# Performance work log

Hardware: AMD Instinct MI355X
Metric: run time of the kernel (lower is better)

The kernel has to match this reference:

```python
import jax, jax.numpy as jnp
import numpy as np

WH, WW = 8, 8
N = WH * WW
DIM = 128
NUM_HEADS = 4
HEAD_DIM = DIM // NUM_HEADS
SCALE = HEAD_DIM ** -0.5


def _relative_position_index():
    coords = np.stack(np.meshgrid(np.arange(WH), np.arange(WW), indexing='ij'))  # (2, Wh, Ww)
    flat = coords.reshape(2, -1)  # (2, N)
    rel = flat[:, :, None] - flat[:, None, :]  # (2, N, N)
    rel = rel.transpose(1, 2, 0)  # (N, N, 2)
    rel[:, :, 0] += WH - 1
    rel[:, :, 1] += WW - 1
    rel[:, :, 0] *= 2 * WW - 1
    return rel.sum(-1)  # (N, N) int

REL_IDX = _relative_position_index()


def setup_inputs() -> dict:
    key = jax.random.key(0)
    ks = jax.random.split(key, 7)
    B_ = 4096
    nW = 64
    table_size = (2 * WH - 1) * (2 * WW - 1)  # 225
    return {
        'x': jax.random.normal(ks[0], (B_, N, DIM), dtype=jnp.float32),
        'mask': jax.random.normal(ks[1], (nW, N, N), dtype=jnp.float32),
        'qkv_w': jax.random.normal(ks[2], (3 * DIM, DIM), dtype=jnp.float32) * 0.02,
        'qkv_b': jnp.zeros((3 * DIM,), dtype=jnp.float32),
        'proj_w': jax.random.normal(ks[3], (DIM, DIM), dtype=jnp.float32) * 0.02,
        'proj_b': jnp.zeros((DIM,), dtype=jnp.float32),
        'bias_table': jax.random.normal(ks[4], (table_size, NUM_HEADS), dtype=jnp.float32) * 0.02,
    }


def reference(x, mask, qkv_w, qkv_b, proj_w, proj_b, bias_table):
    B_, n, C = x.shape
    nW = mask.shape[0]
    qkv = x @ qkv_w.T + qkv_b  # (B_, N, 3C)
    qkv = qkv.reshape(B_, n, 3, NUM_HEADS, HEAD_DIM)
    q = qkv[:, :, 0] * SCALE  # (B_, N, H, hd)
    k = qkv[:, :, 1]
    v = qkv[:, :, 2]
    attn = jnp.einsum('bihd,bjhd->bhij', q, k)  # (B_, H, N, N)
    rel_bias = bias_table[REL_IDX.reshape(-1)].reshape(n, n, NUM_HEADS)
    attn = attn + rel_bias.transpose(2, 0, 1)[None]  # broadcast over B_
    attn = attn.reshape(B_ // nW, nW, NUM_HEADS, n, n) + mask[None, :, None]
    attn = attn.reshape(B_, NUM_HEADS, n, n)
    attn = jax.nn.softmax(attn, axis=-1)
    out = jnp.einsum('bhij,bjhd->bihd', attn, v).reshape(B_, n, C)
    return out @ proj_w.T + proj_b
```

## Files before the change

### kernel.cpp

```cpp
#include <hip/hip_runtime.h>


typedef __bf16 bf16x8 __attribute__((ext_vector_type(8)));
typedef float f32x16 __attribute__((ext_vector_type(16)));

#define MFMA32(a, b, c) __builtin_amdgcn_mfma_f32_32x32x16_bf16(a, b, c, 0, 0, 0)
#define ATT_SCALE 0.17677669529663687f

__device__ __forceinline__ unsigned short f2bf(float f) {
  union { float fv; unsigned int u; } cv; cv.fv = f;
  unsigned int r = cv.u + 0x7FFFu + ((cv.u >> 16) & 1u);
  return (unsigned short)(r >> 16);
}

__global__ __launch_bounds__(256) void convert_weights(
    const float* __restrict__ qkv_w, const float* __restrict__ proj_w,
    unsigned short* __restrict__ wq, unsigned short* __restrict__ wp) {
  int t = blockIdx.x * 256 + threadIdx.x;
  if (t < 384 * 128) wq[t] = f2bf(qkv_w[t]);
  else               wp[t - 384 * 128] = f2bf(proj_w[t - 384 * 128]);
}

__global__ __launch_bounds__(256) void build_cb(
    const float* __restrict__ mask, const float* __restrict__ bias_table,
    float* __restrict__ cb) {
  int t = blockIdx.x * 256 + threadIdx.x;
  int ij = t & 4095;
  int h = (t >> 12) & 3;
  int w = t >> 14;
  int i = ij >> 6, j = ij & 63;
  int ridx = ((i >> 3) - (j >> 3) + 7) * 15 + ((i & 7) - (j & 7) + 7);
  cb[t] = bias_table[ridx * 4 + h] + mask[(w << 12) + ij];
}

__global__ __launch_bounds__(256, 2) void window_attn(
    const float* __restrict__ x, const float* __restrict__ qkv_b,
    const float* __restrict__ proj_b, const unsigned short* __restrict__ wq,
    const unsigned short* __restrict__ wp, const float* __restrict__ cb,
    float* __restrict__ out, int nW) {
  __shared__ unsigned short Xb[64][136];
  __shared__ unsigned short U[4][7424];

  const int tid = threadIdx.x;
  const int h = tid >> 6;
  const int lane = tid & 63;
  const int l31 = lane & 31;
  const int hl = lane >> 5;
  const int b = blockIdx.x;
  const int w = b % nW;

  const float* xb = x + (size_t)b * 8192;
  #pragma unroll
  for (int it = 0; it < 8; ++it) {
    int e = (it * 256 + tid) * 4;
    float4 v = *reinterpret_cast<const float4*>(xb + e);
    ushort4 o;
    o.x = f2bf(v.x); o.y = f2bf(v.y); o.z = f2bf(v.z); o.w = f2bf(v.w);
    *reinterpret_cast<ushort4*>(&Xb[e >> 7][e & 127]) = o;
  }
  __syncthreads();

  unsigned short* qh = &U[h][0];
  unsigned short* kh = &U[h][2560];
  unsigned short* vh = &U[h][5120];
  unsigned short* ph = &U[h][0];

  #pragma unroll
  for (int s = 0; s < 3; ++s) {
    const int c = s * 128 + h * 32 + l31;
    const float bias = qkv_b[c];
    const unsigned short* wrow = wq + (size_t)c * 128 + hl * 8;
    bf16x8 bfr[8];
    #pragma unroll
    for (int kt = 0; kt < 8; ++kt)
      bfr[kt] = *reinterpret_cast<const bf16x8*>(wrow + kt * 16);
    #pragma unroll
    for (int mt = 0; mt < 2; ++mt) {
      f32x16 acc;
      #pragma unroll
      for (int q = 0; q < 16; ++q) acc[q] = 0.0f;
      #pragma unroll
      for (int kt = 0; kt < 8; ++kt) {
        bf16x8 a = *reinterpret_cast<const bf16x8*>(&Xb[mt * 32 + l31][kt * 16 + hl * 8]);
        acc = MFMA32(a, bfr[kt], acc);
      }
      #pragma unroll
      for (int r = 0; r < 16; ++r) {
        int row = (r & 3) + 8 * (r >> 2) + 4 * hl + mt * 32;
        float val = acc[r] + bias;
        if (s == 0)      qh[row * 40 + l31] = f2bf(val * ATT_SCALE);
        else if (s == 1) kh[row * 40 + l31] = f2bf(val);
        else             vh[l31 * 72 + row] = f2bf(val);
      }
    }
  }
  __syncthreads();

  f32x16 sacc[2][2];
  #pragma unroll
  for (int mt = 0; mt < 2; ++mt)
    #pragma unroll
    for (int jt = 0; jt < 2; ++jt)
      #pragma unroll
      for (int q = 0; q < 16; ++q) sacc[mt][jt][q] = 0.0f;
  #pragma unroll
  for (int kt = 0; kt < 2; ++kt) {
    bf16x8 b0 = *reinterpret_cast<const bf16x8*>(&kh[(l31) * 40 + kt * 16 + hl * 8]);
    bf16x8 b1 = *reinterpret_cast<const bf16x8*>(&kh[(32 + l31) * 40 + kt * 16 + hl * 8]);
    #pragma unroll
    for (int mt = 0; mt < 2; ++mt) {
      bf16x8 a = *reinterpret_cast<const bf16x8*>(&qh[(mt * 32 + l31) * 40 + kt * 16 + hl * 8]);
      sacc[mt][0] = MFMA32(a, b0, sacc[mt][0]);
      sacc[mt][1] = MFMA32(a, b1, sacc[mt][1]);
    }
  }

  const float* cbp = cb + (((size_t)w * 4 + h) << 12);
  float rinv[2][16];
  #pragma unroll
  for (int mt = 0; mt < 2; ++mt) {
    #pragma unroll
    for (int r = 0; r < 16; ++r) {
      int row = (r & 3) + 8 * (r >> 2) + 4 * hl + mt * 32;
      float s0 = sacc[mt][0][r] + cbp[row * 64 + l31];
      float s1 = sacc[mt][1][r] + cbp[row * 64 + 32 + l31];
      float m = fmaxf(s0, s1);
      m = fmaxf(m, __shfl_xor(m, 1));
      m = fmaxf(m, __shfl_xor(m, 2));
      m = fmaxf(m, __shfl_xor(m, 4));
      m = fmaxf(m, __shfl_xor(m, 8));
      m = fmaxf(m, __shfl_xor(m, 16));
      float e0 = __expf(s0 - m);
      float e1 = __expf(s1 - m);
      float sum = e0 + e1;
      sum += __shfl_xor(sum, 1);
      sum += __shfl_xor(sum, 2);
      sum += __shfl_xor(sum, 4);
      sum += __shfl_xor(sum, 8);
      sum += __shfl_xor(sum, 16);
      ph[row * 72 + l31] = f2bf(e0);
      ph[row * 72 + 32 + l31] = f2bf(e1);
      rinv[mt][r] = __builtin_amdgcn_rcpf(sum);
    }
  }

  #pragma unroll
  for (int mt = 0; mt < 2; ++mt) {
    f32x16 oacc;
    #pragma unroll
    for (int q = 0; q < 16; ++q) oacc[q] = 0.0f;
    #pragma unroll
    for (int kt = 0; kt < 4; ++kt) {
      bf16x8 a = *reinterpret_cast<const bf16x8*>(&ph[(mt * 32 + l31) * 72 + kt * 16 + hl * 8]);
      bf16x8 bb = *reinterpret_cast<const bf16x8*>(&vh[l31 * 72 + kt * 16 + hl * 8]);
      oacc = MFMA32(a, bb, oacc);
    }
    #pragma unroll
    for (int r = 0; r < 16; ++r) {
      int row = (r & 3) + 8 * (r >> 2) + 4 * hl + mt * 32;
      Xb[row][h * 32 + l31] = f2bf(oacc[r] * rinv[mt][r]);
    }
  }
  __syncthreads();

  {
    const int c = h * 32 + l31;
    const float pb = proj_b[c];
    const unsigned short* wrow = wp + (size_t)c * 128 + hl * 8;
    bf16x8 bfr[8];
    #pragma unroll
    for (int kt = 0; kt < 8; ++kt)
      bfr[kt] = *reinterpret_cast<const bf16x8*>(wrow + kt * 16);
    float* ob = out + (size_t)b * 8192;
    #pragma unroll
    for (int mt = 0; mt < 2; ++mt) {
      f32x16 acc;
      #pragma unroll
      for (int q = 0; q < 16; ++q) acc[q] = 0.0f;
      #pragma unroll
      for (int kt = 0; kt < 8; ++kt) {
        bf16x8 a = *reinterpret_cast<const bf16x8*>(&Xb[mt * 32 + l31][kt * 16 + hl * 8]);
        acc = MFMA32(a, bfr[kt], acc);
      }
      #pragma unroll
      for (int r = 0; r < 16; ++r) {
        int row = (r & 3) + 8 * (r >> 2) + 4 * hl + mt * 32;
        ob[row * 128 + c] = acc[r] + pb;
      }
    }
  }
}

extern "C" void kernel_launch(void* const* d_in, const int* in_sizes, int n_in,
                              void* d_out, int out_size, void* d_ws, size_t ws_size,
                              hipStream_t stream) {
  const float* x          = (const float*)d_in[0];
  const float* mask       = (const float*)d_in[1];
  const float* qkv_w      = (const float*)d_in[2];
  const float* qkv_b      = (const float*)d_in[3];
  const float* proj_w     = (const float*)d_in[4];
  const float* proj_b     = (const float*)d_in[5];
  const float* bias_table = (const float*)d_in[6];
  const int B_ = in_sizes[0] / 8192;
  const int nW = in_sizes[1] / 4096;

  unsigned short* wq = (unsigned short*)d_ws;
  unsigned short* wp = wq + 384 * 128;
  float* cbuf = (float*)((char*)d_ws + 131072);

  convert_weights<<<(384 * 128 + 128 * 128) / 256, 256, 0, stream>>>(qkv_w, proj_w, wq, wp);
  build_cb<<<(nW * 4 * 4096) / 256, 256, 0, stream>>>(mask, bias_table, cbuf);
  window_attn<<<B_, 256, 0, stream>>>(x, qkv_b, proj_b, wq, wp, cbuf, (float*)d_out, nW);
}
```

Measured before the change: 334.9 us.

## Compute transposed scores in registers, drop row-max, fuse prep kernels

```diff
diff --git a/kernel.cpp b/kernel.cpp
--- a/kernel.cpp
+++ b/kernel.cpp
@@ -8,44 +8,72 @@
 #define ATT_SCALE 0.17677669529663687f
 
 __device__ __forceinline__ unsigned short f2bf(float f) {
-  union { float fv; unsigned int u; } cv; cv.fv = f;
-  unsigned int r = cv.u + 0x7FFFu + ((cv.u >> 16) & 1u);
+  union { float fv; unsigned u; } cv; cv.fv = f;
+  unsigned r = cv.u + 0x7FFFu + ((cv.u >> 16) & 1u);
   return (unsigned short)(r >> 16);
 }
-
-__global__ __launch_bounds__(256) void convert_weights(
+__device__ __forceinline__ unsigned pack2(float lo, float hi) {
+  return (unsigned)f2bf(lo) | ((unsigned)f2bf(hi) << 16);
+}
+__device__ __forceinline__ bf16x8 frag_from(unsigned a, unsigned b, unsigned c, unsigned d) {
+  union { unsigned u[4]; bf16x8 v; } t;
+  t.u[0] = a; t.u[1] = b; t.u[2] = c; t.u[3] = d;
+  return t.v;
+}
+
+#define BUILD_FRAG(frag, arr, kt) {                                        \
+  unsigned pA0 = arr[(kt) >> 1][4 * ((kt) & 1) + 0];                       \
+  unsigned pA1 = arr[(kt) >> 1][4 * ((kt) & 1) + 1];                       \
+  unsigned pB0 = arr[(kt) >> 1][4 * ((kt) & 1) + 2];                       \
+  unsigned pB1 = arr[(kt) >> 1][4 * ((kt) & 1) + 3];                       \
+  unsigned t0 = hl ? pA0 : pB0, t1 = hl ? pA1 : pB1;                       \
+  unsigned r0 = (unsigned)__shfl_xor((int)t0, 32);                         \
+  unsigned r1 = (unsigned)__shfl_xor((int)t1, 32);                         \
+  frag = hl ? frag_from(r0, r1, pB0, pB1) : frag_from(pA0, pA1, r0, r1); }
+
+__global__ __launch_bounds__(256) void prep(
+    const float* __restrict__ mask, const float* __restrict__ bias_table,
     const float* __restrict__ qkv_w, const float* __restrict__ proj_w,
-    unsigned short* __restrict__ wq, unsigned short* __restrict__ wp) {
-  int t = blockIdx.x * 256 + threadIdx.x;
-  if (t < 384 * 128) wq[t] = f2bf(qkv_w[t]);
-  else               wp[t - 384 * 128] = f2bf(proj_w[t - 384 * 128]);
-}
-
-__global__ __launch_bounds__(256) void build_cb(
-    const float* __restrict__ mask, const float* __restrict__ bias_table,
-    float* __restrict__ cb) {
-  int t = blockIdx.x * 256 + threadIdx.x;
-  int ij = t & 4095;
-  int h = (t >> 12) & 3;
-  int w = t >> 14;
-  int i = ij >> 6, j = ij & 63;
-  int ridx = ((i >> 3) - (j >> 3) + 7) * 15 + ((i & 7) - (j & 7) + 7);
-  cb[t] = bias_table[ridx * 4 + h] + mask[(w << 12) + ij];
-}
-
-__global__ __launch_bounds__(256, 2) void window_attn(
+    float* __restrict__ cbT, unsigned short* __restrict__ wq,
+    unsigned short* __restrict__ wp) {
+  int blk = blockIdx.x;
+  if (blk < 256) {
+    __shared__ float ms[64][65];
+    int w = blk >> 2, h = blk & 3;
+    const float* mw = mask + ((size_t)w << 12);
+    #pragma unroll
+    for (int it = 0; it < 16; ++it) {
+      int idx = it * 256 + threadIdx.x;
+      ms[idx >> 6][idx & 63] = mw[idx];
+    }
+    __syncthreads();
+    float* cw = cbT + ((size_t)blk << 12);
+    #pragma unroll
+    for (int it = 0; it < 16; ++it) {
+      int idx = it * 256 + threadIdx.x;
+      int j = idx >> 6, i = idx & 63;
+      int ridx = ((i >> 3) - (j >> 3) + 7) * 15 + ((i & 7) - (j & 7) + 7);
+      cw[idx] = ms[i][j] + bias_table[ridx * 4 + h];
+    }
+  } else {
+    int t = (blk - 256) * 2048 + threadIdx.x;
+    #pragma unroll
+    for (int it = 0; it < 8; ++it, t += 256) {
+      if (t < 384 * 128) wq[t] = f2bf(qkv_w[t]);
+      else               wp[t - 384 * 128] = f2bf(proj_w[t - 384 * 128]);
+    }
+  }
+}
+
+__global__ __launch_bounds__(256, 4) void window_attn(
     const float* __restrict__ x, const float* __restrict__ qkv_b,
     const float* __restrict__ proj_b, const unsigned short* __restrict__ wq,
-    const unsigned short* __restrict__ wp, const float* __restrict__ cb,
+    const unsigned short* __restrict__ wp, const float* __restrict__ cbT,
     float* __restrict__ out, int nW) {
-  __shared__ unsigned short Xb[64][136];
-  __shared__ unsigned short U[4][7424];
+  __shared__ unsigned short L[20480];
 
   const int tid = threadIdx.x;
-  const int h = tid >> 6;
-  const int lane = tid & 63;
-  const int l31 = lane & 31;
-  const int hl = lane >> 5;
+  const int h = tid >> 6, lane = tid & 63, l31 = lane & 31, hl = lane >> 5;
   const int b = blockIdx.x;
   const int w = b % nW;
 
@@ -53,112 +81,125 @@
   #pragma unroll
   for (int it = 0; it < 8; ++it) {
     int e = (it * 256 + tid) * 4;
-    float4 v = *reinterpret_cast<const float4*>(xb + e);
-    ushort4 o;
-    o.x = f2bf(v.x); o.y = f2bf(v.y); o.z = f2bf(v.z); o.w = f2bf(v.w);
-    *reinterpret_cast<ushort4*>(&Xb[e >> 7][e & 127]) = o;
-  }
-  __syncthreads();
-
-  unsigned short* qh = &U[h][0];
-  unsigned short* kh = &U[h][2560];
-  unsigned short* vh = &U[h][5120];
-  unsigned short* ph = &U[h][0];
-
-  #pragma unroll
-  for (int s = 0; s < 3; ++s) {
-    const int c = s * 128 + h * 32 + l31;
-    const float bias = qkv_b[c];
-    const unsigned short* wrow = wq + (size_t)c * 128 + hl * 8;
-    bf16x8 bfr[8];
+    float4 v4 = *reinterpret_cast<const float4*>(xb + e);
+    uint2 u; u.x = pack2(v4.x, v4.y); u.y = pack2(v4.z, v4.w);
+    *reinterpret_cast<uint2*>(&L[(e >> 7) * 136 + (e & 127)]) = u;
+  }
+  __syncthreads();
+
+  unsigned qpk[2][8], kpk[2][8], vpk[2][8];
+  #pragma unroll
+  for (int mt = 0; mt < 2; ++mt) {
+    bf16x8 aF[8];
     #pragma unroll
     for (int kt = 0; kt < 8; ++kt)
-      bfr[kt] = *reinterpret_cast<const bf16x8*>(wrow + kt * 16);
-    #pragma unroll
-    for (int mt = 0; mt < 2; ++mt) {
+      aF[kt] = *reinterpret_cast<const bf16x8*>(&L[(mt * 32 + l31) * 136 + kt * 16 + hl * 8]);
+    #pragma unroll
+    for (int s = 0; s < 3; ++s) {
+      const int c = s * 128 + h * 32 + l31;
+      const float bias = qkv_b[c];
+      const unsigned short* wrow = wq + c * 128 + hl * 8;
       f32x16 acc;
       #pragma unroll
       for (int q = 0; q < 16; ++q) acc[q] = 0.0f;
       #pragma unroll
       for (int kt = 0; kt < 8; ++kt) {
-        bf16x8 a = *reinterpret_cast<const bf16x8*>(&Xb[mt * 32 + l31][kt * 16 + hl * 8]);
-        acc = MFMA32(a, bfr[kt], acc);
-      }
+        bf16x8 bF = *reinterpret_cast<const bf16x8*>(wrow + kt * 16);
+        acc = MFMA32(aF[kt], bF, acc);
+      }
+      #pragma unroll
+      for (int p = 0; p < 8; ++p) {
+        float lo = acc[2 * p] + bias, hi = acc[2 * p + 1] + bias;
+        if (s == 0) { lo *= ATT_SCALE; hi *= ATT_SCALE; qpk[mt][p] = pack2(lo, hi); }
+        else if (s == 1) kpk[mt][p] = pack2(lo, hi);
+        else             vpk[mt][p] = pack2(lo, hi);
+      }
+    }
+  }
+  __syncthreads();
+
+  unsigned short* qh = &L[h * 5120];
+  unsigned short* kh = qh + 2560;
+  #pragma unroll
+  for (int mt = 0; mt < 2; ++mt)
+    #pragma unroll
+    for (int p = 0; p < 8; ++p) {
+      int row = ((2 * p) & 3) + 8 * (p >> 1) + 4 * hl + 32 * mt;
+      qh[row * 40 + l31]       = (unsigned short)(qpk[mt][p] & 0xFFFF);
+      qh[(row + 1) * 40 + l31] = (unsigned short)(qpk[mt][p] >> 16);
+      kh[row * 40 + l31]       = (unsigned short)(kpk[mt][p] & 0xFFFF);
+      kh[(row + 1) * 40 + l31] = (unsigned short)(kpk[mt][p] >> 16);
+    }
+
+  f32x16 sacc[2][2];
+  const float* cbp = cbT + (((size_t)(w * 4 + h)) << 12);
+  #pragma unroll
+  for (int mtj = 0; mtj < 2; ++mtj)
+    #pragma unroll
+    for (int r = 0; r < 16; ++r) {
+      int j = (r & 3) + 8 * (r >> 2) + 4 * hl + 32 * mtj;
+      sacc[mtj][0][r] = cbp[j * 64 + l31];
+      sacc[mtj][1][r] = cbp[j * 64 + 32 + l31];
+    }
+
+  #pragma unroll
+  for (int kt = 0; kt < 2; ++kt) {
+    bf16x8 a0 = *reinterpret_cast<const bf16x8*>(&kh[l31 * 40 + kt * 16 + hl * 8]);
+    bf16x8 a1 = *reinterpret_cast<const bf16x8*>(&kh[(32 + l31) * 40 + kt * 16 + hl * 8]);
+    bf16x8 b0 = *reinterpret_cast<const bf16x8*>(&qh[l31 * 40 + kt * 16 + hl * 8]);
+    bf16x8 b1 = *reinterpret_cast<const bf16x8*>(&qh[(32 + l31) * 40 + kt * 16 + hl * 8]);
+    sacc[0][0] = MFMA32(a0, b0, sacc[0][0]);
+    sacc[0][1] = MFMA32(a0, b1, sacc[0][1]);
+    sacc[1][0] = MFMA32(a1, b0, sacc[1][0]);
+    sacc[1][1] = MFMA32(a1, b1, sacc[1][1]);
+  }
+
+  float rinv[2];
+  unsigned epk[2][2][8];
+  #pragma unroll
+  for (int nti = 0; nti < 2; ++nti) {
+    float e[2][16];
+    float ssum = 0.0f;
+    #pragma unroll
+    for (int mtj = 0; mtj < 2; ++mtj)
       #pragma unroll
       for (int r = 0; r < 16; ++r) {
-        int row = (r & 3) + 8 * (r >> 2) + 4 * hl + mt * 32;
-        float val = acc[r] + bias;
-        if (s == 0)      qh[row * 40 + l31] = f2bf(val * ATT_SCALE);
-        else if (s == 1) kh[row * 40 + l31] = f2bf(val);
-        else             vh[l31 * 72 + row] = f2bf(val);
-      }
-    }
-  }
-  __syncthreads();
-
-  f32x16 sacc[2][2];
-  #pragma unroll
-  for (int mt = 0; mt < 2; ++mt)
-    #pragma unroll
-    for (int jt = 0; jt < 2; ++jt)
-      #pragma unroll
-      for (int q = 0; q < 16; ++q) sacc[mt][jt][q] = 0.0f;
-  #pragma unroll
-  for (int kt = 0; kt < 2; ++kt) {
-    bf16x8 b0 = *reinterpret_cast<const bf16x8*>(&kh[(l31) * 40 + kt * 16 + hl * 8]);
-    bf16x8 b1 = *reinterpret_cast<const bf16x8*>(&kh[(32 + l31) * 40 + kt * 16 + hl * 8]);
-    #pragma unroll
-    for (int mt = 0; mt < 2; ++mt) {
-      bf16x8 a = *reinterpret_cast<const bf16x8*>(&qh[(mt * 32 + l31) * 40 + kt * 16 + hl * 8]);
-      sacc[mt][0] = MFMA32(a, b0, sacc[mt][0]);
-      sacc[mt][1] = MFMA32(a, b1, sacc[mt][1]);
-    }
-  }
-
-  const float* cbp = cb + (((size_t)w * 4 + h) << 12);
-  float rinv[2][16];
-  #pragma unroll
-  for (int mt = 0; mt < 2; ++mt) {
-    #pragma unroll
-    for (int r = 0; r < 16; ++r) {
-      int row = (r & 3) + 8 * (r >> 2) + 4 * hl + mt * 32;
-      float s0 = sacc[mt][0][r] + cbp[row * 64 + l31];
-      float s1 = sacc[mt][1][r] + cbp[row * 64 + 32 + l31];
-      float m = fmaxf(s0, s1);
-      m = fmaxf(m, __shfl_xor(m, 1));
-      m = fmaxf(m, __shfl_xor(m, 2));
-      m = fmaxf(m, __shfl_xor(m, 4));
-      m = fmaxf(m, __shfl_xor(m, 8));
-      m = fmaxf(m, __shfl_xor(m, 16));
-      float e0 = __expf(s0 - m);
-      float e1 = __expf(s1 - m);
-      float sum = e0 + e1;
-      sum += __shfl_xor(sum, 1);
-      sum += __shfl_xor(sum, 2);
-      sum += __shfl_xor(sum, 4);
-      sum += __shfl_xor(sum, 8);
-      sum += __shfl_xor(sum, 16);
-      ph[row * 72 + l31] = f2bf(e0);
-      ph[row * 72 + 32 + l31] = f2bf(e1);
-      rinv[mt][r] = __builtin_amdgcn_rcpf(sum);
-    }
-  }
-
-  #pragma unroll
-  for (int mt = 0; mt < 2; ++mt) {
-    f32x16 oacc;
-    #pragma unroll
-    for (int q = 0; q < 16; ++q) oacc[q] = 0.0f;
-    #pragma unroll
-    for (int kt = 0; kt < 4; ++kt) {
-      bf16x8 a = *reinterpret_cast<const bf16x8*>(&ph[(mt * 32 + l31) * 72 + kt * 16 + hl * 8]);
-      bf16x8 bb = *reinterpret_cast<const bf16x8*>(&vh[l31 * 72 + kt * 16 + hl * 8]);
-      oacc = MFMA32(a, bb, oacc);
-    }
-    #pragma unroll
-    for (int r = 0; r < 16; ++r) {
-      int row = (r & 3) + 8 * (r >> 2) + 4 * hl + mt * 32;
-      Xb[row][h * 32 + l31] = f2bf(oacc[r] * rinv[mt][r]);
+        float ev = __expf(sacc[mtj][nti][r]);
+        e[mtj][r] = ev; ssum += ev;
+      }
+    ssum += __shfl_xor(ssum, 32);
+    rinv[nti] = __builtin_amdgcn_rcpf(ssum);
+    #pragma unroll
+    for (int mtj = 0; mtj < 2; ++mtj)
+      #pragma unroll
+      for (int p = 0; p < 8; ++p)
+        epk[nti][mtj][p] = pack2(e[mtj][2 * p], e[mtj][2 * p + 1]);
+  }
+
+  f32x16 oacc[2];
+  #pragma unroll
+  for (int nti = 0; nti < 2; ++nti)
+    #pragma unroll
+    for (int q = 0; q < 16; ++q) oacc[nti][q] = 0.0f;
+  #pragma unroll
+  for (int kt = 0; kt < 4; ++kt) {
+    bf16x8 av;  BUILD_FRAG(av, vpk, kt);
+    bf16x8 bp0; BUILD_FRAG(bp0, epk[0], kt);
+    bf16x8 bp1; BUILD_FRAG(bp1, epk[1], kt);
+    oacc[0] = MFMA32(av, bp0, oacc[0]);
+    oacc[1] = MFMA32(av, bp1, oacc[1]);
+  }
+
+  __syncthreads();
+
+  #pragma unroll
+  for (int nti = 0; nti < 2; ++nti) {
+    int i = nti * 32 + l31;
+    #pragma unroll
+    for (int p = 0; p < 8; ++p) {
+      int d = ((2 * p) & 3) + 8 * (p >> 1) + 4 * hl;
+      unsigned u = pack2(oacc[nti][2 * p] * rinv[nti], oacc[nti][2 * p + 1] * rinv[nti]);
+      *reinterpret_cast<unsigned*>(&L[i * 136 + h * 32 + d]) = u;
     }
   }
   __syncthreads();
@@ -166,7 +207,7 @@
   {
     const int c = h * 32 + l31;
     const float pb = proj_b[c];
-    const unsigned short* wrow = wp + (size_t)c * 128 + hl * 8;
+    const unsigned short* wrow = wp + c * 128 + hl * 8;
     bf16x8 bfr[8];
     #pragma unroll
     for (int kt = 0; kt < 8; ++kt)
@@ -179,12 +220,12 @@
       for (int q = 0; q < 16; ++q) acc[q] = 0.0f;
       #pragma unroll
       for (int kt = 0; kt < 8; ++kt) {
-        bf16x8 a = *reinterpret_cast<const bf16x8*>(&Xb[mt * 32 + l31][kt * 16 + hl * 8]);
-        acc = MFMA32(a, bfr[kt], acc);
+        bf16x8 aF = *reinterpret_cast<const bf16x8*>(&L[(mt * 32 + l31) * 136 + kt * 16 + hl * 8]);
+        acc = MFMA32(aF, bfr[kt], acc);
       }
       #pragma unroll
       for (int r = 0; r < 16; ++r) {
-        int row = (r & 3) + 8 * (r >> 2) + 4 * hl + mt * 32;
+        int row = (r & 3) + 8 * (r >> 2) + 4 * hl + 32 * mt;
         ob[row * 128 + c] = acc[r] + pb;
       }
     }
@@ -206,9 +247,8 @@
 
   unsigned short* wq = (unsigned short*)d_ws;
   unsigned short* wp = wq + 384 * 128;
-  float* cbuf = (float*)((char*)d_ws + 131072);
-
-  convert_weights<<<(384 * 128 + 128 * 128) / 256, 256, 0, stream>>>(qkv_w, proj_w, wq, wp);
-  build_cb<<<(nW * 4 * 4096) / 256, 256, 0, stream>>>(mask, bias_table, cbuf);
-  window_attn<<<B_, 256, 0, stream>>>(x, qkv_b, proj_b, wq, wp, cbuf, (float*)d_out, nW);
-}
+  float* cbT = (float*)((char*)d_ws + 131072);
+
+  prep<<<288, 256, 0, stream>>>(mask, bias_table, qkv_w, proj_w, cbT, wq, wp);
+  window_attn<<<B_, 256, 0, stream>>>(x, qkv_b, proj_b, wq, wp, cbT, (float*)d_out, nW);
+}
```

Result: slower. 379.1 us (+13.2%).
